# Kernel tuning notes

Measured on AMD Instinct MI355X. Metric: run time of the kernel, lower is better.

## Reference

```python
import jax, jax.numpy as jnp
import numpy as np

B, S, D, H, DH = 2, 1024, 1024, 16, 64  # batch, seq, dim_model, heads, dim_head


def setup_inputs() -> dict:
    key = jax.random.key(0)
    ks = jax.random.split(key, 9)
    def W(k):
        return jax.random.normal(k, (D, D), jnp.float32) * 0.02
    z = jnp.zeros((D,), jnp.float32)
    return {
        "x": jax.random.normal(ks[0], (B, S, D), jnp.float32),
        "rel_pos_emb": jax.random.normal(ks[1], (B, S, D), jnp.float32),
        "padding_mask": jnp.zeros((B, S), jnp.int32),
        "Wq": W(ks[2]), "bq": z,
        "Wk": W(ks[3]), "bk": z,
        "Wv": W(ks[4]), "bv": z,
        "Wqr": W(ks[5]), "bqr": z,
        "Wkr": W(ks[6]), "bkr": z,
        "Wc": W(ks[7]), "bc": z,
    }


def reference(x, rel_pos_emb, padding_mask, Wq, bq, Wk, bk, Wv, bv, Wqr, bqr, Wkr, bkr, Wc, bc):
    b, s, d = x.shape

    def proj(t, W_, b_):  # (b,s,D) -> (b,H,s,DH)
        return (t @ W_.T + b_).reshape(b, s, H, DH).transpose(0, 2, 1, 3)

    q = proj(x, Wq, bq)
    k = proj(x, Wk, bk)
    v = proj(x, Wv, bv)
    qr = proj(rel_pos_emb, Wqr, bqr)
    kr = proj(rel_pos_emb, Wkr, bkr)

    # relative position index: clamp(i - j + MAX_REL_POS/2, 0, MAX_REL_POS-1), MAX_REL_POS = S
    idx = jnp.arange(s)
    pos = jnp.clip(idx[:, None] - idx[None, :] + s // 2, 0, s - 1)  # (s,s) int
    pos_b = jnp.broadcast_to(pos[None, None], (b, H, s, s))

    c2c = jnp.einsum('bhid,bhjd->bhij', q, k)
    c2p_att = jnp.einsum('bhid,bhjd->bhij', q, kr)
    c2p = jnp.take_along_axis(c2p_att, pos_b, axis=-1)   # gather along last dim
    p2c_att = jnp.einsum('bhid,bhjd->bhij', qr, k)
    p2c = jnp.take_along_axis(p2c_att, pos_b, axis=-2)   # gather along query dim

    scale = jnp.sqrt(jnp.asarray(3 * DH, jnp.float32))
    scores = (c2c + c2p + p2c) / scale
    scores = jnp.where(padding_mask[:, None, None, :] == 1, -jnp.inf, scores)
    attn = jax.nn.softmax(scores, axis=-1)  # dropout is identity in eval

    out = jnp.einsum('bhij,bhjd->bhid', attn, v)
    out = out.transpose(0, 2, 1, 3).reshape(b, s, H * DH)
    return out @ Wc.T + bc
```

## Files before the change

### kernel.cpp

```cpp
#include <hip/hip_runtime.h>

typedef unsigned short u16;
typedef unsigned int   u32;
typedef __bf16 bf16x8 __attribute__((ext_vector_type(8)));
typedef float  f32x4  __attribute__((ext_vector_type(4)));

__device__ __forceinline__ float b2f(u16 s) { return __uint_as_float(((u32)s) << 16); }
__device__ __forceinline__ u16 f2b(float f) {
  u32 x = __float_as_uint(f);
  return (u16)((x + 0x7FFFu + ((x >> 16) & 1u)) >> 16);
}

#if __has_builtin(__builtin_amdgcn_exp2f)
#define EXP2(x) __builtin_amdgcn_exp2f(x)
#else
#define EXP2(x) exp2f(x)
#endif

template <int C>
__device__ __forceinline__ u32 dppu(u32 s) {
  return (u32)__builtin_amdgcn_update_dpp((int)s, (int)s, C, 0xF, 0xF, false);
}
__device__ __forceinline__ float red_sum16(float x) {
  x += __uint_as_float(dppu<0x128>(__float_as_uint(x)));
  x += __uint_as_float(dppu<0x124>(__float_as_uint(x)));
  x += __uint_as_float(dppu<0x122>(__float_as_uint(x)));
  x += __uint_as_float(dppu<0x121>(__float_as_uint(x)));
  return x;
}

union U16x8 { uint4 u; u16 s[8]; };

__device__ __forceinline__ uint4 cvt8(const float4 a, const float4 b) {
  U16x8 r;
  r.s[0] = f2b(a.x); r.s[1] = f2b(a.y); r.s[2] = f2b(a.z); r.s[3] = f2b(a.w);
  r.s[4] = f2b(b.x); r.s[5] = f2b(b.y); r.s[6] = f2b(b.z); r.s[7] = f2b(b.w);
  return r.u;
}

typedef __attribute__((address_space(3))) u32 lds_u32;
typedef const __attribute__((address_space(1))) u32 glb_u32;
__device__ __forceinline__ void gld16(const u16* gp, u16* lp) {
  __builtin_amdgcn_global_load_lds((glb_u32*)gp, (lds_u32*)lp, 16, 0, 0);
}

struct CvtArgs { const float* s[8]; u16* d[8]; int n[8]; };

__global__ __launch_bounds__(256) void cvt_bf16(CvtArgs c) {
  const int t = blockIdx.y;
  const int i = (blockIdx.x * 256 + threadIdx.x) * 8;
  if (i >= c.n[t]) return;
  const float4 a = *(const float4*)(c.s[t] + i);
  const float4 b = *(const float4*)(c.s[t] + i + 4);
  *(uint4*)(c.d[t] + i) = cvt8(a, b);
}

struct GemmBArgs { const u16* A[5]; const u16* W[5]; const float* Bi[5]; void* C[5]; int vtz; };

template <int BM, int BN, bool OUT_F32>
__global__ __launch_bounds__(256) void gemm_lds(GemmBArgs g, int M, int N, int K) {
  const int z = blockIdx.z;
  const u16* __restrict__ A = g.A[z];
  const u16* __restrict__ W = g.W[z];
  const float* __restrict__ Bi = g.Bi[z];

  const int m0 = blockIdx.y * BM, n0 = blockIdx.x * BN;
  const int tid = threadIdx.x, wv = tid >> 6, lane = tid & 63;
  const int wm = wv >> 1, wn = wv & 1;
  const int lr = lane & 15, lq = lane >> 4;
  constexpr int MT = BM / 32;
  constexpr int NT = BN / 32;

  __shared__ u16 As[BM * 64];
  __shared__ u16 Ws[BN * 64];

  const f32x4 vzero = {0.f, 0.f, 0.f, 0.f};
  f32x4 acc[MT][NT];
#pragma unroll
  for (int i = 0; i < MT; ++i)
#pragma unroll
    for (int j = 0; j < NT; ++j) acc[i][j] = vzero;

  const int srow = lane >> 3;
  const int sc   = (lane & 7) ^ srow;

  for (int kb = 0; kb < K; kb += 64) {
    __syncthreads();
#pragma unroll
    for (int t = 0; t < MT; ++t) {
      const u16* gp = A + (size_t)(m0 + t * 32 + wv * 8 + srow) * K + kb + sc * 8;
      gld16(gp, As + (t * 32 + wv * 8) * 64 + lane * 8);
    }
#pragma unroll
    for (int t = 0; t < NT; ++t) {
      const u16* gp = W + (size_t)(n0 + t * 32 + wv * 8 + srow) * K + kb + sc * 8;
      gld16(gp, Ws + (t * 32 + wv * 8) * 64 + lane * 8);
    }
    __syncthreads();
#pragma unroll
    for (int kk = 0; kk < 2; ++kk) {
      bf16x8 af[MT], bw[NT];
#pragma unroll
      for (int mt = 0; mt < MT; ++mt) {
        const int row = wm * (BM / 2) + mt * 16 + lr;
        af[mt] = *(const bf16x8*)&As[row * 64 + (((kk << 2) | lq) ^ (row & 7)) * 8];
      }
#pragma unroll
      for (int nt = 0; nt < NT; ++nt) {
        const int row = wn * (BN / 2) + nt * 16 + lr;
        bw[nt] = *(const bf16x8*)&Ws[row * 64 + (((kk << 2) | lq) ^ (row & 7)) * 8];
      }
#pragma unroll
      for (int mt = 0; mt < MT; ++mt)
#pragma unroll
        for (int nt = 0; nt < NT; ++nt)
          acc[mt][nt] = __builtin_amdgcn_mfma_f32_16x16x32_bf16(af[mt], bw[nt], acc[mt][nt], 0, 0, 0);
    }
  }

#pragma unroll
  for (int mt = 0; mt < MT; ++mt) {
#pragma unroll
    for (int nt = 0; nt < NT; ++nt) {
      const int col = n0 + wn * (BN / 2) + nt * 16 + lr;
      const float bia = Bi[col];
      const int row0 = m0 + wm * (BM / 2) + mt * 16 + lq * 4;
      if (OUT_F32) {
#pragma unroll
        for (int r = 0; r < 4; ++r)
          ((float*)g.C[z])[(size_t)(row0 + r) * N + col] = acc[mt][nt][r] + bia;
      } else if (z == g.vtz) {
        ushort4 pk;
        pk.x = f2b(acc[mt][nt][0] + bia); pk.y = f2b(acc[mt][nt][1] + bia);
        pk.z = f2b(acc[mt][nt][2] + bia); pk.w = f2b(acc[mt][nt][3] + bia);
        const int bb = row0 >> 10, s0 = row0 & 1023;
        *(ushort4*)((u16*)g.C[z] + ((size_t)bb << 20) + ((size_t)col << 10) + s0) = pk;
      } else {
#pragma unroll
        for (int r = 0; r < 4; ++r)
          ((u16*)g.C[z])[(size_t)(row0 + r) * N + col] = f2b(acc[mt][nt][r] + bia);
      }
    }
  }
}

struct GemmArgs { const void* A[5]; const float* W[5]; const float* Bi[5]; void* C[5]; int vtz; };

template <bool A_F32, bool OUT_F32>
__global__ __launch_bounds__(256) void gemm5(GemmArgs g, int M, int N, int K) {
  const int z = blockIdx.z;
  const float* __restrict__ Wf = g.W[z];
  const float* __restrict__ Bi = g.Bi[z];

  const int m0 = blockIdx.y * 128, n0 = blockIdx.x * 128;
  const int tid = threadIdx.x;
  const int wv = tid >> 6, lane = tid & 63;
  const int wm = wv >> 1, wn = wv & 1;
  const int lr = lane & 15, lq = lane >> 4;

  __shared__ alignas(16) u16 As[128][64];
  __shared__ alignas(16) u16 Ws[128][64];

  const f32x4 vzero = {0.f, 0.f, 0.f, 0.f};
  f32x4 acc[4][4];
#pragma unroll
  for (int i = 0; i < 4; ++i)
#pragma unroll
    for (int j = 0; j < 4; ++j) acc[i][j] = vzero;

  const int srow = tid >> 1;
  const int sc0  = (tid & 1) * 32;
  const float* pw = Wf + (size_t)(n0 + srow) * K + sc0;
  const float* paf = A_F32 ? ((const float*)g.A[z] + (size_t)(m0 + srow) * K + sc0) : nullptr;
  const u16*   pab = A_F32 ? nullptr : ((const u16*)g.A[z] + (size_t)(m0 + srow) * K + sc0);

  for (int k0 = 0; k0 < K; k0 += 64) {
#pragma unroll
    for (int u_ = 0; u_ < 4; ++u_) {
      const float4 w0 = *(const float4*)(pw + k0 + u_ * 8);
      const float4 w1 = *(const float4*)(pw + k0 + u_ * 8 + 4);
      *(uint4*)&Ws[srow][sc0 + u_ * 8] = cvt8(w0, w1);
      if (A_F32) {
        const float4 a0 = *(const float4*)(paf + k0 + u_ * 8);
        const float4 a1 = *(const float4*)(paf + k0 + u_ * 8 + 4);
        *(uint4*)&As[srow][sc0 + u_ * 8] = cvt8(a0, a1);
      } else {
        *(uint4*)&As[srow][sc0 + u_ * 8] = *(const uint4*)(pab + k0 + u_ * 8);
      }
    }
    __syncthreads();
#pragma unroll
    for (int kk = 0; kk < 2; ++kk) {
      bf16x8 af[4], bfr[4];
#pragma unroll
      for (int mt = 0; mt < 4; ++mt)
        af[mt] = *(const bf16x8*)&As[wm * 64 + mt * 16 + lr][kk * 32 + lq * 8];
#pragma unroll
      for (int nt = 0; nt < 4; ++nt)
        bfr[nt] = *(const bf16x8*)&Ws[wn * 64 + nt * 16 + lr][kk * 32 + lq * 8];
#pragma unroll
      for (int mt = 0; mt < 4; ++mt)
#pragma unroll
        for (int nt = 0; nt < 4; ++nt)
          acc[mt][nt] = __builtin_amdgcn_mfma_f32_16x16x32_bf16(af[mt], bfr[nt], acc[mt][nt], 0, 0, 0);
    }
    __syncthreads();
  }

#pragma unroll
  for (int mt = 0; mt < 4; ++mt) {
#pragma unroll
    for (int nt = 0; nt < 4; ++nt) {
      const int col = n0 + wn * 64 + nt * 16 + lr;
      const float bia = Bi[col];
      const int row0 = m0 + wm * 64 + mt * 16 + lq * 4;
      if (OUT_F32) {
#pragma unroll
        for (int r = 0; r < 4; ++r)
          ((float*)g.C[z])[(size_t)(row0 + r) * N + col] = acc[mt][nt][r] + bia;
      } else if (z == g.vtz) {
        ushort4 pk;
        pk.x = f2b(acc[mt][nt][0] + bia); pk.y = f2b(acc[mt][nt][1] + bia);
        pk.z = f2b(acc[mt][nt][2] + bia); pk.w = f2b(acc[mt][nt][3] + bia);
        const int bb = row0 >> 10, s0 = row0 & 1023;
        *(ushort4*)((u16*)g.C[z] + ((size_t)bb << 20) + ((size_t)col << 10) + s0) = pk;
      } else {
#pragma unroll
        for (int r = 0; r < 4; ++r)
          ((u16*)g.C[z])[(size_t)(row0 + r) * N + col] = f2b(acc[mt][nt][r] + bia);
      }
    }
  }
}

__global__ __launch_bounds__(256, 2) void attn_wave(
    const u16* __restrict__ q, const u16* __restrict__ k,
    const u16* __restrict__ vT, const u16* __restrict__ qr,
    const u16* __restrict__ kr, const int* __restrict__ pmask,
    u16* __restrict__ ao) {
  constexpr int S = 1024, Dm = 1024;
  constexpr int GP = 37;
  constexpr int PBP = 36;
  constexpr int WLDS = 11776;

  __shared__ alignas(16) char smem[4 * WLDS];

  const int bx = blockIdx.x;
  const int bh = bx & 31, it = bx >> 5;
  const int bb = bh >> 4, h = bh & 15;
  const int i0 = it * 32;

  const int tid = threadIdx.x;
  const int wv = tid >> 6, lane = tid & 63;
  const int lq = lane >> 4, lr = lane & 15;

  char* wbase = smem + wv * WLDS;
  float* G1f = (float*)wbase;
  float* G2f = (float*)(wbase + 4736);
  u16*   Pb  = (u16*)(wbase + 9472);

  const u16* qb  = q  + ((size_t)bb << 20) + h * 64;
  const u16* kb  = k  + ((size_t)bb << 20) + h * 64;
  const u16* qrb = qr + ((size_t)bb << 20) + h * 64;
  const u16* krb = kr + ((size_t)bb << 20) + h * 64;
  const u16* vtb = vT + ((size_t)bb << 20) + ((size_t)h << 16);
  const int* pmb = pmask + ((size_t)bb << 10);

  const float kscale = 1.44269504088896f / 13.856406460551018f;

  bf16x8 qf[2][2];
#pragma unroll
  for (int mt = 0; mt < 2; ++mt)
#pragma unroll
    for (int kk = 0; kk < 2; ++kk)
      qf[mt][kk] = *(const bf16x8*)(qb + (size_t)(i0 + mt * 16 + lr) * Dm + kk * 32 + lq * 8);

  const f32x4 vzero = {0.f, 0.f, 0.f, 0.f};
  f32x4 o[2][4];
#pragma unroll
  for (int mt = 0; mt < 2; ++mt)
#pragma unroll
    for (int nd = 0; nd < 4; ++nd) o[mt][nd] = vzero;
  float lst[2][4];
#pragma unroll
  for (int mt = 0; mt < 2; ++mt)
#pragma unroll
    for (int r = 0; r < 4; ++r) lst[mt][r] = 0.f;

#pragma unroll 1
  for (int t8 = 0; t8 < 8; ++t8) {
    const int j0 = (wv + t8 * 4) * 32;
    const int pb_ = i0 - j0 + 481;

    bf16x8 kf[2][2], vf[4];
#pragma unroll
    for (int nt = 0; nt < 2; ++nt) {
      const u16* kp = kb + (size_t)(j0 + nt * 16 + lr) * Dm + lq * 8;
      kf[nt][0] = *(const bf16x8*)kp;
      kf[nt][1] = *(const bf16x8*)(kp + 32);
    }
#pragma unroll
    for (int n4 = 0; n4 < 4; ++n4)
      vf[n4] = *(const bf16x8*)(vtb + (size_t)(n4 * 16 + lr) * S + j0 + lq * 8);
    const int mv0 = pmb[j0 + lr], mv1 = pmb[j0 + 16 + lr];

    f32x4 cc[2][2];
#pragma unroll
    for (int mt = 0; mt < 2; ++mt)
#pragma unroll
      for (int nt = 0; nt < 2; ++nt) {
        f32x4 a = vzero;
        a = __builtin_amdgcn_mfma_f32_16x16x32_bf16(qf[mt][0], kf[nt][0], a, 0, 0, 0);
        a = __builtin_amdgcn_mfma_f32_16x16x32_bf16(qf[mt][1], kf[nt][1], a, 0, 0, 0);
        cc[mt][nt] = a;
      }

#pragma unroll
    for (int n4 = 0; n4 < 4; ++n4) {
      int p = pb_ + n4 * 16 + lr;
      p = p < 0 ? 0 : (p > 1023 ? 1023 : p);
      const u16* kp = krb + (size_t)p * Dm + lq * 8;
      const u16* qp = qrb + (size_t)p * Dm + lq * 8;
      const bf16x8 kr0 = *(const bf16x8*)kp;
      const bf16x8 kr1 = *(const bf16x8*)(kp + 32);
      const bf16x8 qr0 = *(const bf16x8*)qp;
      const bf16x8 qr1 = *(const bf16x8*)(qp + 32);
      const int tb = n4 * 16 + lr;
#pragma unroll
      for (int mt = 0; mt < 2; ++mt) {
        f32x4 a = vzero;
        a = __builtin_amdgcn_mfma_f32_16x16x32_bf16(qf[mt][0], kr0, a, 0, 0, 0);
        a = __builtin_amdgcn_mfma_f32_16x16x32_bf16(qf[mt][1], kr1, a, 0, 0, 0);
#pragma unroll
        for (int r = 0; r < 4; ++r) {
          const int arow = mt * 16 + lq * 4 + r;
          int u = tb - arow;
          u = u < -2 ? -2 : (u > 34 ? 34 : u);
          G1f[2 + arow * GP + u] = a[r];
        }
      }
#pragma unroll
      for (int mt = 0; mt < 2; ++mt) {
        f32x4 g = vzero;
        g = __builtin_amdgcn_mfma_f32_16x16x32_bf16(kf[mt][0], qr0, g, 0, 0, 0);
        g = __builtin_amdgcn_mfma_f32_16x16x32_bf16(kf[mt][1], qr1, g, 0, 0, 0);
#pragma unroll
        for (int r = 0; r < 4; ++r) {
          const int brow = mt * 16 + lq * 4 + r;
          int u = tb + brow - 31;
          u = u < -2 ? -2 : (u > 34 ? 34 : u);
          G2f[2 + brow * GP + u] = g[r];
        }
      }
    }

#pragma unroll
    for (int mt = 0; mt < 2; ++mt) {
#pragma unroll
      for (int r = 0; r < 4; ++r) {
        const int a_ = mt * 16 + lq * 4 + r;
        float s0 = cc[mt][0][r] + G1f[2 + a_ * GP + 31 - lr] + G2f[2 + lr * GP + a_];
        float s1 = cc[mt][1][r] + G1f[2 + a_ * GP + 15 - lr] + G2f[2 + (16 + lr) * GP + a_];
        s0 = mv0 ? -1e30f : s0 * kscale;
        s1 = mv1 ? -1e30f : s1 * kscale;
        const float p0 = EXP2(s0);
        const float p1 = EXP2(s1);
        lst[mt][r] += p0 + p1;
        Pb[a_ * PBP + lr]      = f2b(p0);
        Pb[a_ * PBP + 16 + lr] = f2b(p1);
      }
    }

#pragma unroll
    for (int mt = 0; mt < 2; ++mt) {
      union { uint2 u2[2]; bf16x8 v; } pr;
      const u16* prow = Pb + (mt * 16 + lr) * PBP + lq * 8;
      pr.u2[0] = *(const uint2*)prow;
      pr.u2[1] = *(const uint2*)(prow + 4);
#pragma unroll
      for (int nd = 0; nd < 4; ++nd)
        o[mt][nd] = __builtin_amdgcn_mfma_f32_16x16x32_bf16(pr.v, vf[nd], o[mt][nd], 0, 0, 0);
    }
  }

  {
    float* Orm = (float*)wbase;
    float* llw = (float*)(wbase + 8192);
#pragma unroll
    for (int mt = 0; mt < 2; ++mt)
#pragma unroll
      for (int nd = 0; nd < 4; ++nd)
#pragma unroll
        for (int r = 0; r < 4; ++r)
          Orm[(mt * 16 + lq * 4 + r) * 64 + nd * 16 + lr] = o[mt][nd][r];
#pragma unroll
    for (int mt = 0; mt < 2; ++mt)
#pragma unroll
      for (int r = 0; r < 4; ++r) {
        const float rl = red_sum16(lst[mt][r]);
        if (lr == 0) llw[mt * 16 + lq * 4 + r] = rl;
      }
  }
  __syncthreads();
  {
    const int a_ = tid >> 3, d0 = (tid & 7) * 8;
    float L = 0.f, acc[8];
#pragma unroll
    for (int d = 0; d < 8; ++d) acc[d] = 0.f;
#pragma unroll
    for (int w = 0; w < 4; ++w) {
      const char* wb = smem + w * WLDS;
      L += *(const float*)(wb + 8192 + a_ * 4);
      const float* Ow = (const float*)wb + a_ * 64 + d0;
#pragma unroll
      for (int d = 0; d < 8; ++d) acc[d] += Ow[d];
    }
    const float inv = 1.f / L;
    U16x8 pk;
#pragma unroll
    for (int d = 0; d < 8; ++d) pk.s[d] = f2b(acc[d] * inv);
    *(uint4*)(ao + ((size_t)((bb << 10) + i0 + a_) << 10) + (h << 6) + d0) = pk.u;
  }
}

extern "C" void kernel_launch(void* const* d_in, const int* in_sizes, int n_in,
                              void* d_out, int out_size, void* d_ws, size_t ws_size,
                              hipStream_t stream) {
  const float* x   = (const float*)d_in[0];
  const float* rpe = (const float*)d_in[1];
  const int*   pm  = (const int*)d_in[2];
  const float* Wq  = (const float*)d_in[3];  const float* bq  = (const float*)d_in[4];
  const float* Wk  = (const float*)d_in[5];  const float* bk  = (const float*)d_in[6];
  const float* Wv  = (const float*)d_in[7];  const float* bv  = (const float*)d_in[8];
  const float* Wqr = (const float*)d_in[9];  const float* bqr = (const float*)d_in[10];
  const float* Wkr = (const float*)d_in[11]; const float* bkr = (const float*)d_in[12];
  const float* Wc  = (const float*)d_in[13]; const float* bc  = (const float*)d_in[14];

  const size_t NE = (size_t)2 * 1024 * 1024;
  const size_t WE = (size_t)1024 * 1024;
  u16* ws = (u16*)d_ws;

  if (ws_size >= (10 * NE + 6 * WE) * sizeof(u16)) {
    u16* q   = ws;          u16* k   = ws + NE;     u16* vT  = ws + 2 * NE;
    u16* qr  = ws + 3 * NE; u16* kr  = ws + 4 * NE;
    u16* xb  = ws + 5 * NE;
    u16* ao  = ws + 5 * NE;
    u16* rpb = ws + 6 * NE;
    u16* wb  = ws + 7 * NE;
    u16* Wqb = wb;           u16* Wkb = wb + WE;     u16* Wvb = wb + 2 * WE;
    u16* Wqrb= wb + 3 * WE;  u16* Wkrb= wb + 4 * WE; u16* Wcb = wb + 5 * WE;

    CvtArgs c;
    c.s[0] = x;   c.d[0] = xb;   c.n[0] = (int)NE;
    c.s[1] = rpe; c.d[1] = rpb;  c.n[1] = (int)NE;
    c.s[2] = Wq;  c.d[2] = Wqb;  c.n[2] = (int)WE;
    c.s[3] = Wk;  c.d[3] = Wkb;  c.n[3] = (int)WE;
    c.s[4] = Wv;  c.d[4] = Wvb;  c.n[4] = (int)WE;
    c.s[5] = Wqr; c.d[5] = Wqrb; c.n[5] = (int)WE;
    c.s[6] = Wkr; c.d[6] = Wkrb; c.n[6] = (int)WE;
    c.s[7] = Wc;  c.d[7] = Wcb;  c.n[7] = (int)WE;
    cvt_bf16<<<dim3(1024, 8), 256, 0, stream>>>(c);

    GemmBArgs g;
    g.A[0] = xb;  g.W[0] = Wqb;  g.Bi[0] = bq;  g.C[0] = q;
    g.A[1] = xb;  g.W[1] = Wkb;  g.Bi[1] = bk;  g.C[1] = k;
    g.A[2] = xb;  g.W[2] = Wvb;  g.Bi[2] = bv;  g.C[2] = vT;
    g.A[3] = rpb; g.W[3] = Wqrb; g.Bi[3] = bqr; g.C[3] = qr;
    g.A[4] = rpb; g.W[4] = Wkrb; g.Bi[4] = bkr; g.C[4] = kr;
    g.vtz = 2;
    gemm_lds<128, 128, false><<<dim3(8, 16, 5), 256, 0, stream>>>(g, 2048, 1024, 1024);

    attn_wave<<<dim3(1024), 256, 0, stream>>>(q, k, vT, qr, kr, pm, ao);

    GemmBArgs g2;
    for (int i = 0; i < 5; ++i) { g2.A[i] = ao; g2.W[i] = Wcb; g2.Bi[i] = bc; g2.C[i] = d_out; }
    g2.vtz = -1;
    gemm_lds<64, 64, true><<<dim3(16, 32, 1), 256, 0, stream>>>(g2, 2048, 1024, 1024);
  } else {
    if (ws_size < 6 * NE * sizeof(u16)) return;
    u16* q  = ws;          u16* k  = ws + NE;     u16* vT = ws + 2 * NE;
    u16* qr = ws + 3 * NE; u16* kr = ws + 4 * NE; u16* ao = ws + 5 * NE;

    GemmArgs g;
    g.A[0] = x;   g.W[0] = Wq;  g.Bi[0] = bq;  g.C[0] = q;
    g.A[1] = x;   g.W[1] = Wk;  g.Bi[1] = bk;  g.C[1] = k;
    g.A[2] = x;   g.W[2] = Wv;  g.Bi[2] = bv;  g.C[2] = vT;
    g.A[3] = rpe; g.W[3] = Wqr; g.Bi[3] = bqr; g.C[3] = qr;
    g.A[4] = rpe; g.W[4] = Wkr; g.Bi[4] = bkr; g.C[4] = kr;
    g.vtz = 2;
    gemm5<true, false><<<dim3(8, 16, 5), 256, 0, stream>>>(g, 2048, 1024, 1024);

    attn_wave<<<dim3(1024), 256, 0, stream>>>(q, k, vT, qr, kr, pm, ao);

    GemmArgs g2;
    for (int i = 0; i < 5; ++i) { g2.A[i] = ao; g2.W[i] = Wc; g2.Bi[i] = bc; g2.C[i] = d_out; }
    g2.vtz = -1;
    gemm5<false, true><<<dim3(8, 16, 1), 256, 0, stream>>>(g2, 2048, 1024, 1024);
  }
}
```

Before: 235.8 us.

## Halve attention query tile to 16 rows and double grid size

```diff
diff --git a/kernel.cpp b/kernel.cpp
--- a/kernel.cpp
+++ b/kernel.cpp
@@ -239,16 +239,17 @@
     const u16* __restrict__ kr, const int* __restrict__ pmask,
     u16* __restrict__ ao) {
   constexpr int S = 1024, Dm = 1024;
-  constexpr int GP = 37;
+  constexpr int G1P = 37;
+  constexpr int G2P = 21;
   constexpr int PBP = 36;
-  constexpr int WLDS = 11776;
+  constexpr int WLDS = 6272;
 
   __shared__ alignas(16) char smem[4 * WLDS];
 
   const int bx = blockIdx.x;
   const int bh = bx & 31, it = bx >> 5;
   const int bb = bh >> 4, h = bh & 15;
-  const int i0 = it * 32;
+  const int i0 = it * 16;
 
   const int tid = threadIdx.x;
   const int wv = tid >> 6, lane = tid & 63;
@@ -256,8 +257,8 @@
 
   char* wbase = smem + wv * WLDS;
   float* G1f = (float*)wbase;
-  float* G2f = (float*)(wbase + 4736);
-  u16*   Pb  = (u16*)(wbase + 9472);
+  float* G2f = (float*)(wbase + 2384);
+  u16*   Pb  = (u16*)(wbase + 5088);
 
   const u16* qb  = q  + ((size_t)bb << 20) + h * 64;
   const u16* kb  = k  + ((size_t)bb << 20) + h * 64;
@@ -268,55 +269,44 @@
 
   const float kscale = 1.44269504088896f / 13.856406460551018f;
 
-  bf16x8 qf[2][2];
-#pragma unroll
-  for (int mt = 0; mt < 2; ++mt)
-#pragma unroll
-    for (int kk = 0; kk < 2; ++kk)
-      qf[mt][kk] = *(const bf16x8*)(qb + (size_t)(i0 + mt * 16 + lr) * Dm + kk * 32 + lq * 8);
+  bf16x8 qf[2];
+#pragma unroll
+  for (int kk = 0; kk < 2; ++kk)
+    qf[kk] = *(const bf16x8*)(qb + (size_t)(i0 + lr) * Dm + kk * 32 + lq * 8);
 
   const f32x4 vzero = {0.f, 0.f, 0.f, 0.f};
-  f32x4 o[2][4];
-#pragma unroll
-  for (int mt = 0; mt < 2; ++mt)
-#pragma unroll
-    for (int nd = 0; nd < 4; ++nd) o[mt][nd] = vzero;
-  float lst[2][4];
-#pragma unroll
-  for (int mt = 0; mt < 2; ++mt)
-#pragma unroll
-    for (int r = 0; r < 4; ++r) lst[mt][r] = 0.f;
+  f32x4 o[4];
+#pragma unroll
+  for (int nd = 0; nd < 4; ++nd) o[nd] = vzero;
+  float lst[4];
+#pragma unroll
+  for (int r = 0; r < 4; ++r) lst[r] = 0.f;
 
 #pragma unroll 1
   for (int t8 = 0; t8 < 8; ++t8) {
     const int j0 = (wv + t8 * 4) * 32;
     const int pb_ = i0 - j0 + 481;
 
-    bf16x8 kf[2][2], vf[4];
+    bf16x8 kf[2][2];
 #pragma unroll
     for (int nt = 0; nt < 2; ++nt) {
       const u16* kp = kb + (size_t)(j0 + nt * 16 + lr) * Dm + lq * 8;
       kf[nt][0] = *(const bf16x8*)kp;
       kf[nt][1] = *(const bf16x8*)(kp + 32);
     }
-#pragma unroll
-    for (int n4 = 0; n4 < 4; ++n4)
-      vf[n4] = *(const bf16x8*)(vtb + (size_t)(n4 * 16 + lr) * S + j0 + lq * 8);
     const int mv0 = pmb[j0 + lr], mv1 = pmb[j0 + 16 + lr];
 
-    f32x4 cc[2][2];
-#pragma unroll
-    for (int mt = 0; mt < 2; ++mt)
-#pragma unroll
-      for (int nt = 0; nt < 2; ++nt) {
-        f32x4 a = vzero;
-        a = __builtin_amdgcn_mfma_f32_16x16x32_bf16(qf[mt][0], kf[nt][0], a, 0, 0, 0);
-        a = __builtin_amdgcn_mfma_f32_16x16x32_bf16(qf[mt][1], kf[nt][1], a, 0, 0, 0);
-        cc[mt][nt] = a;
-      }
-
-#pragma unroll
-    for (int n4 = 0; n4 < 4; ++n4) {
+    f32x4 cc[2];
+#pragma unroll
+    for (int nt = 0; nt < 2; ++nt) {
+      f32x4 a = vzero;
+      a = __builtin_amdgcn_mfma_f32_16x16x32_bf16(qf[0], kf[nt][0], a, 0, 0, 0);
+      a = __builtin_amdgcn_mfma_f32_16x16x32_bf16(qf[1], kf[nt][1], a, 0, 0, 0);
+      cc[nt] = a;
+    }
+
+#pragma unroll
+    for (int n4 = 0; n4 < 3; ++n4) {
       int p = pb_ + n4 * 16 + lr;
       p = p < 0 ? 0 : (p > 1023 ? 1023 : p);
       const u16* kp = krb + (size_t)p * Dm + lq * 8;
@@ -326,17 +316,16 @@
       const bf16x8 qr0 = *(const bf16x8*)qp;
       const bf16x8 qr1 = *(const bf16x8*)(qp + 32);
       const int tb = n4 * 16 + lr;
-#pragma unroll
-      for (int mt = 0; mt < 2; ++mt) {
+      {
         f32x4 a = vzero;
-        a = __builtin_amdgcn_mfma_f32_16x16x32_bf16(qf[mt][0], kr0, a, 0, 0, 0);
-        a = __builtin_amdgcn_mfma_f32_16x16x32_bf16(qf[mt][1], kr1, a, 0, 0, 0);
+        a = __builtin_amdgcn_mfma_f32_16x16x32_bf16(qf[0], kr0, a, 0, 0, 0);
+        a = __builtin_amdgcn_mfma_f32_16x16x32_bf16(qf[1], kr1, a, 0, 0, 0);
 #pragma unroll
         for (int r = 0; r < 4; ++r) {
-          const int arow = mt * 16 + lq * 4 + r;
+          const int arow = lq * 4 + r;
           int u = tb - arow;
           u = u < -2 ? -2 : (u > 34 ? 34 : u);
-          G1f[2 + arow * GP + u] = a[r];
+          G1f[2 + arow * G1P + u] = a[r];
         }
       }
 #pragma unroll
@@ -348,78 +337,75 @@
         for (int r = 0; r < 4; ++r) {
           const int brow = mt * 16 + lq * 4 + r;
           int u = tb + brow - 31;
-          u = u < -2 ? -2 : (u > 34 ? 34 : u);
-          G2f[2 + brow * GP + u] = g[r];
+          u = u < -2 ? -2 : (u > 18 ? 18 : u);
+          G2f[2 + brow * G2P + u] = g[r];
         }
       }
     }
 
 #pragma unroll
-    for (int mt = 0; mt < 2; ++mt) {
-#pragma unroll
-      for (int r = 0; r < 4; ++r) {
-        const int a_ = mt * 16 + lq * 4 + r;
-        float s0 = cc[mt][0][r] + G1f[2 + a_ * GP + 31 - lr] + G2f[2 + lr * GP + a_];
-        float s1 = cc[mt][1][r] + G1f[2 + a_ * GP + 15 - lr] + G2f[2 + (16 + lr) * GP + a_];
-        s0 = mv0 ? -1e30f : s0 * kscale;
-        s1 = mv1 ? -1e30f : s1 * kscale;
-        const float p0 = EXP2(s0);
-        const float p1 = EXP2(s1);
-        lst[mt][r] += p0 + p1;
-        Pb[a_ * PBP + lr]      = f2b(p0);
-        Pb[a_ * PBP + 16 + lr] = f2b(p1);
-      }
-    }
-
-#pragma unroll
-    for (int mt = 0; mt < 2; ++mt) {
+    for (int r = 0; r < 4; ++r) {
+      const int a_ = lq * 4 + r;
+      float s0 = cc[0][r] + G1f[2 + a_ * G1P + 31 - lr] + G2f[2 + lr * G2P + a_];
+      float s1 = cc[1][r] + G1f[2 + a_ * G1P + 15 - lr] + G2f[2 + (16 + lr) * G2P + a_];
+      s0 = mv0 ? -1e30f : s0 * kscale;
+      s1 = mv1 ? -1e30f : s1 * kscale;
+      const float p0 = EXP2(s0);
+      const float p1 = EXP2(s1);
+      lst[r] += p0 + p1;
+      Pb[a_ * PBP + lr]      = f2b(p0);
+      Pb[a_ * PBP + 16 + lr] = f2b(p1);
+    }
+
+    bf16x8 vf[4];
+#pragma unroll
+    for (int n4 = 0; n4 < 4; ++n4)
+      vf[n4] = *(const bf16x8*)(vtb + (size_t)(n4 * 16 + lr) * S + j0 + lq * 8);
+
+    {
       union { uint2 u2[2]; bf16x8 v; } pr;
-      const u16* prow = Pb + (mt * 16 + lr) * PBP + lq * 8;
+      const u16* prow = Pb + lr * PBP + lq * 8;
       pr.u2[0] = *(const uint2*)prow;
       pr.u2[1] = *(const uint2*)(prow + 4);
 #pragma unroll
       for (int nd = 0; nd < 4; ++nd)
-        o[mt][nd] = __builtin_amdgcn_mfma_f32_16x16x32_bf16(pr.v, vf[nd], o[mt][nd], 0, 0, 0);
+        o[nd] = __builtin_amdgcn_mfma_f32_16x16x32_bf16(pr.v, vf[nd], o[nd], 0, 0, 0);
     }
   }
 
   {
     float* Orm = (float*)wbase;
-    float* llw = (float*)(wbase + 8192);
-#pragma unroll
-    for (int mt = 0; mt < 2; ++mt)
-#pragma unroll
-      for (int nd = 0; nd < 4; ++nd)
-#pragma unroll
-        for (int r = 0; r < 4; ++r)
-          Orm[(mt * 16 + lq * 4 + r) * 64 + nd * 16 + lr] = o[mt][nd][r];
-#pragma unroll
-    for (int mt = 0; mt < 2; ++mt)
-#pragma unroll
-      for (int r = 0; r < 4; ++r) {
-        const float rl = red_sum16(lst[mt][r]);
-        if (lr == 0) llw[mt * 16 + lq * 4 + r] = rl;
-      }
+    float* llw = (float*)(wbase + 4096);
+#pragma unroll
+    for (int nd = 0; nd < 4; ++nd)
+#pragma unroll
+      for (int r = 0; r < 4; ++r)
+        Orm[(lq * 4 + r) * 64 + nd * 16 + lr] = o[nd][r];
+#pragma unroll
+    for (int r = 0; r < 4; ++r) {
+      const float rl = red_sum16(lst[r]);
+      if (lr == 0) llw[lq * 4 + r] = rl;
+    }
   }
   __syncthreads();
   {
-    const int a_ = tid >> 3, d0 = (tid & 7) * 8;
-    float L = 0.f, acc[8];
-#pragma unroll
-    for (int d = 0; d < 8; ++d) acc[d] = 0.f;
+    const int a_ = tid >> 4, d0 = (tid & 15) * 4;
+    float L = 0.f, acc[4];
+#pragma unroll
+    for (int d = 0; d < 4; ++d) acc[d] = 0.f;
 #pragma unroll
     for (int w = 0; w < 4; ++w) {
       const char* wb = smem + w * WLDS;
-      L += *(const float*)(wb + 8192 + a_ * 4);
+      L += *(const float*)(wb + 4096 + a_ * 4);
       const float* Ow = (const float*)wb + a_ * 64 + d0;
 #pragma unroll
-      for (int d = 0; d < 8; ++d) acc[d] += Ow[d];
+      for (int d = 0; d < 4; ++d) acc[d] += Ow[d];
     }
     const float inv = 1.f / L;
-    U16x8 pk;
-#pragma unroll
-    for (int d = 0; d < 8; ++d) pk.s[d] = f2b(acc[d] * inv);
-    *(uint4*)(ao + ((size_t)((bb << 10) + i0 + a_) << 10) + (h << 6) + d0) = pk.u;
+    ushort4 pk;
+    pk.x = f2b(acc[0] * inv); pk.y = f2b(acc[1] * inv);
+    pk.z = f2b(acc[2] * inv); pk.w = f2b(acc[3] * inv);
+    *(ushort4*)(ao + ((size_t)((bb << 10) + i0 + a_) << 10) + (h << 6) + d0) = pk;
   }
 }
 
@@ -470,7 +456,7 @@
     g.vtz = 2;
     gemm_lds<128, 128, false><<<dim3(8, 16, 5), 256, 0, stream>>>(g, 2048, 1024, 1024);
 
-    attn_wave<<<dim3(1024), 256, 0, stream>>>(q, k, vT, qr, kr, pm, ao);
+    attn_wave<<<dim3(2048), 256, 0, stream>>>(q, k, vT, qr, kr, pm, ao);
 
     GemmBArgs g2;
     for (int i = 0; i < 5; ++i) { g2.A[i] = ao; g2.W[i] = Wcb; g2.Bi[i] = bc; g2.C[i] = d_out; }
@@ -490,7 +476,7 @@
     g.vtz = 2;
     gemm5<true, false><<<dim3(8, 16, 5), 256, 0, stream>>>(g, 2048, 1024, 1024);
 
-    attn_wave<<<dim3(1024), 256, 0, stream>>>(q, k, vT, qr, kr, pm, ao);
+    attn_wave<<<dim3(2048), 256, 0, stream>>>(q, k, vT, qr, kr, pm, ao);
 
     GemmArgs g2;
     for (int i = 0; i < 5; ++i) { g2.A[i] = ao; g2.W[i] = Wc; g2.Bi[i] = bc; g2.C[i] = d_out; }
```

After: 298.0 us. 26.4% more time.
